# Optimization experiments

Measured on AMD Instinct MI355X. Metric: run time of the kernel, lower is better.

The kernel has to match this reference:

```python
import jax, jax.numpy as jnp
import numpy as np


def setup_inputs() -> dict:
    key = jax.random.key(0)
    ks = jax.random.split(key, 6)
    B, S, D, F, E = 4, 2048, 512, 2048, 8
    scale = 0.02
    return {
        "x": jax.random.normal(ks[0], (B, S, D), dtype=jnp.float32),
        "gate_w": jax.random.normal(ks[1], (D, E), dtype=jnp.float32) * scale,
        "w1": jax.random.normal(ks[2], (E, D, F), dtype=jnp.float32) * scale,
        "b1": jax.random.normal(ks[3], (E, F), dtype=jnp.float32) * scale,
        "w2": jax.random.normal(ks[4], (E, F, D), dtype=jnp.float32) * scale,
        "b2": jax.random.normal(ks[5], (E, D), dtype=jnp.float32) * scale,
    }


TOP_K = 2


def reference(x, gate_w, w1, b1, w2, b2):
    E = w1.shape[0]
    orig_shape = x.shape
    xr = x.reshape(-1, x.shape[-1])              # [T, D]

    # Router
    logits = xr @ gate_w                          # [T, E]
    probs = jax.nn.softmax(logits, axis=-1)
    mean_probs = probs.mean(axis=0)               # [E]
    load_balance_loss = E * jnp.sum(mean_probs * mean_probs)

    topw, topi = jax.lax.top_k(probs, TOP_K)      # [T, K]
    topw = topw / jnp.sum(topw, axis=-1, keepdims=True)

    # Per-token combine weight per expert: sum over top-k slots of weight * one-hot
    combine = jnp.sum(jax.nn.one_hot(topi, E, dtype=xr.dtype) * topw[..., None], axis=1)  # [T, E]

    # Dense per-expert FFN (equivalent math to the permute/slice dispatch:
    # each selected token gets expert_e(x) scaled by its normalized router weight).
    hidden = jax.nn.gelu(jnp.einsum("td,edf->etf", xr, w1) + b1[:, None, :], approximate=False)  # [E, T, F]
    outs = jnp.einsum("etf,efd->etd", hidden, w2) + b2[:, None, :]                               # [E, T, D]

    y = jnp.einsum("etd,te->td", outs, combine)   # [T, D]
    return y.reshape(orig_shape), load_balance_loss
```

## Files before the change

### kernel.cpp

```cpp
#include <hip/hip_runtime.h>
#include <stdint.h>

#define T_TOKENS 8192
#define D_DIM 512
#define F_DIM 2048
#define E_NUM 8

typedef short short8 __attribute__((ext_vector_type(8)));
typedef float f32x4 __attribute__((ext_vector_type(4)));

__device__ __forceinline__ unsigned short f2bf(float f) {
    union { float f; unsigned int u; } c; c.f = f;
    unsigned int u = c.u;
    unsigned int r = (u + 0x7fffu + ((u >> 16) & 1u)) >> 16;
    return (unsigned short)r;
}
__device__ __forceinline__ unsigned int pack2(float a, float b) {
    return (unsigned int)f2bf(a) | ((unsigned int)f2bf(b) << 16);
}
__device__ __forceinline__ float gelu_fast(float h) {
    float a = h * fmaf(h * h, -0.0713548162f, -1.5957691216f);
    return h / (1.f + __expf(a));
}

#define SLOT_CAP 17408
#define WS_COUNT 0
#define WS_PROBS 512
#define WS_TOK   16384
#define WS_WGT   (WS_TOK + E_NUM * T_TOKENS * 4)
#define WS_W1B   (1ull << 20)
#define WS_W2B   (WS_W1B + 16777216ull)
#define WS_XG    (WS_W2B + 16777216ull)
#define WS_HG    (WS_XG + (unsigned long long)SLOT_CAP * D_DIM * 2)

__device__ __forceinline__ void expert_off(const int* __restrict__ count, int e,
                                           int& off_e, int& cnt_e) {
    int off = 0, ce = 0;
#pragma unroll
    for (int i = 0; i < E_NUM; ++i) {
        int c = count[i];
        if (i == e) ce = c;
        if (i < e) off += (c + 127) & ~127;
    }
    off_e = off; cnt_e = ce;
}

__global__ __launch_bounds__(256) void moe_pre(
    const float* __restrict__ w1, const float* __restrict__ w2,
    const float* __restrict__ x,  const float* __restrict__ gw,
    unsigned short* __restrict__ w1b, unsigned short* __restrict__ w2b,
    int* __restrict__ count, float* __restrict__ probs_g,
    int* __restrict__ tok_list, float* __restrict__ wgt_list,
    float* __restrict__ y)
{
    int tid = threadIdx.x;

    if (blockIdx.x < 8192) {
        __shared__ float ts[32][65];
        {
            size_t gid = (size_t)blockIdx.x * 256 + tid;
            ((float2*)y)[gid] = make_float2(0.f, 0.f);
        }
        if (blockIdx.x == 0 && tid < E_NUM) { count[tid] = 0; probs_g[tid] = 0.f; }

        int b = blockIdx.x;
        bool is2 = b >= 4096;
        int o = is2 ? b - 4096 : b;
        int e = o >> 9, r = o & 511;
        int N  = is2 ? 512 : 2048;
        int Ks = is2 ? 64 : 16;
        int ng, ks;
        if (!is2) { ng = r & 31; ks = r >> 5; }
        else      { ng = r & 7;  ks = r >> 3; }

        const float* src = (is2 ? w2 : w1) + ((size_t)e << 20) + (size_t)(ks * 32) * N + ng * 64;
        int row = tid >> 3, c4 = (tid & 7) * 4;
        f32x4 v0 = *(const f32x4*)(src + (size_t)row * N + c4);
        f32x4 v1 = *(const f32x4*)(src + (size_t)row * N + c4 + 32);
        *(f32x4*)&ts[row][c4] = v0;
        *(f32x4*)&ts[row][c4 + 32] = v1;
        __syncthreads();

        int f = tid >> 6, L = tid & 63, q = L >> 4, n = L & 15;
        float v[8];
#pragma unroll
        for (int j = 0; j < 8; ++j) v[j] = ts[q * 8 + j][f * 16 + n];
        uint4 pk;
        pk.x = pack2(v[0], v[1]); pk.y = pack2(v[2], v[3]);
        pk.z = pack2(v[4], v[5]); pk.w = pack2(v[6], v[7]);
        size_t fraglane = ((size_t)((e * (N / 16) + ng * 4 + f) * Ks + ks)) * 64 + L;
        unsigned short* dst = (is2 ? w2b : w1b) + fraglane * 8;
        *(uint4*)dst = pk;
        return;
    }

    int rbx = blockIdx.x - 8192;
    __shared__ float pprob[E_NUM];
    __shared__ int   lcnt[E_NUM];
    __shared__ int   gbase[E_NUM];
    __shared__ int   ltok[E_NUM][64];
    __shared__ float lwgt[E_NUM][64];

    if (tid < E_NUM) { pprob[tid] = 0.f; lcnt[tid] = 0; }
    __syncthreads();

    int wv = tid >> 6, lane = tid & 63;

    float gr[64];
    {
        const f32x4* gp = (const f32x4*)(gw + lane * 64);
#pragma unroll
        for (int i = 0; i < 16; ++i) *(f32x4*)&gr[i * 4] = gp[i];
    }

    float wps[E_NUM];
#pragma unroll
    for (int e = 0; e < E_NUM; ++e) wps[e] = 0.f;

#pragma unroll 1
    for (int i = 0; i < 8; ++i) {
        int t = rbx * 32 + wv * 8 + i;
        const float* xp = x + (size_t)t * D_DIM + lane * 8;
        f32x4 x0 = *(const f32x4*)xp;
        f32x4 x1 = *(const f32x4*)(xp + 4);
        float xv[8] = { x0.x, x0.y, x0.z, x0.w, x1.x, x1.y, x1.z, x1.w };
        float acc[E_NUM];
#pragma unroll
        for (int e = 0; e < E_NUM; ++e) acc[e] = 0.f;
#pragma unroll
        for (int j = 0; j < 8; ++j)
#pragma unroll
            for (int e = 0; e < E_NUM; ++e) acc[e] += xv[j] * gr[j * 8 + e];
#pragma unroll
        for (int off = 1; off < 64; off <<= 1)
#pragma unroll
            for (int e = 0; e < E_NUM; ++e) acc[e] += __shfl_xor(acc[e], off);

        float m = acc[0];
#pragma unroll
        for (int e = 1; e < E_NUM; ++e) m = fmaxf(m, acc[e]);
        float p[E_NUM], s = 0.f;
#pragma unroll
        for (int e = 0; e < E_NUM; ++e) { p[e] = __expf(acc[e] - m); s += p[e]; }
        float inv = 1.f / s;
#pragma unroll
        for (int e = 0; e < E_NUM; ++e) { p[e] *= inv; wps[e] += p[e]; }

        int e1 = 0;
#pragma unroll
        for (int e = 1; e < E_NUM; ++e) if (p[e] > p[e1]) e1 = e;
        int e2 = (e1 == 0) ? 1 : 0;
#pragma unroll
        for (int e = 0; e < E_NUM; ++e) if (e != e1 && p[e] > p[e2]) e2 = e;

        if (lane == 0) {
            float invw = 1.f / (p[e1] + p[e2]);
            int s1 = atomicAdd(&lcnt[e1], 1); ltok[e1][s1] = t; lwgt[e1][s1] = p[e1] * invw;
            int s2 = atomicAdd(&lcnt[e2], 1); ltok[e2][s2] = t; lwgt[e2][s2] = p[e2] * invw;
        }
    }
    if (lane == 0) {
#pragma unroll
        for (int e = 0; e < E_NUM; ++e) atomicAdd(&pprob[e], wps[e]);
    }
    __syncthreads();
    if (tid < E_NUM) {
        gbase[tid] = atomicAdd(&count[tid], lcnt[tid]);
        atomicAdd(&probs_g[tid], pprob[tid]);
    }
    __syncthreads();
    int ee = tid >> 5;
    for (int ss = tid & 31; ss < lcnt[ee]; ss += 32) {
        int dst = ee * T_TOKENS + gbase[ee] + ss;
        tok_list[dst] = ltok[ee][ss];
        wgt_list[dst] = lwgt[ee][ss];
    }
}

__global__ __launch_bounds__(256) void moe_gather(
    const float* __restrict__ x, const int* __restrict__ count,
    const int* __restrict__ tok_list, unsigned short* __restrict__ Xg,
    const float* __restrict__ probs_g, float* __restrict__ y)
{
    if (blockIdx.x == 0 && threadIdx.x == 0) {
        float s = 0.f;
#pragma unroll
        for (int i = 0; i < E_NUM; ++i) {
            float m = probs_g[i] / (float)T_TOKENS;
            s += m * m;
        }
        y[(size_t)T_TOKENS * D_DIM] = (float)E_NUM * s;
    }

    int e = blockIdx.x & 7, tile = blockIdx.x >> 3;
    int off_e, cnt;
    expert_off(count, e, off_e, cnt);
    int padcnt = (cnt + 127) & ~127;
    if (tile * 64 >= padcnt) return;

    int tid = threadIdx.x;
    int tl = tid >> 2;
    int kq = tid & 3;
    int slot = tile * 64 + tl;
    bool valid = slot < cnt;
    int tok = valid ? tok_list[e * T_TOKENS + slot] : 0;
    const float* xr = x + (size_t)tok * D_DIM + kq * 128;
    int base16 = ((off_e + tile * 64) >> 4) + (tl >> 4);
    int mlane = tl & 15;

#pragma unroll 4
    for (int g = 0; g < 16; ++g) {
        uint4 pk;
        if (valid) {
            f32x4 v0 = *(const f32x4*)(xr + g * 8);
            f32x4 v1 = *(const f32x4*)(xr + g * 8 + 4);
            pk.x = pack2(v0.x, v0.y); pk.y = pack2(v0.z, v0.w);
            pk.z = pack2(v1.x, v1.y); pk.w = pack2(v1.z, v1.w);
        } else {
            pk.x = 0; pk.y = 0; pk.z = 0; pk.w = 0;
        }
        int kb = kq * 4 + (g >> 2);
        int lane = mlane + 16 * (g & 3);
        *(uint4*)(Xg + ((size_t)(base16 * 16 + kb) * 64 + lane) * 8) = pk;
    }
}

__global__ __launch_bounds__(256) void moe_gemm1(
    const unsigned short* __restrict__ Xg, const unsigned short* __restrict__ w1b,
    const float* __restrict__ b1, const int* __restrict__ count,
    unsigned short* __restrict__ Hg)
{
    int e = blockIdx.x & 7;
    int r = blockIdx.x >> 3;
    int mt = r >> 4, nt = r & 15;
    int off_e, cnt;
    expert_off(count, e, off_e, cnt);
    if (mt * 128 >= cnt) return;

    __shared__ unsigned short us[4][64][72];

    int tid = threadIdx.x;
    int wv = tid >> 6, lane = tid & 63;
    int wh = wv >> 1, nh = wv & 1;
    int q = lane >> 4, n = lane & 15;

    int slot16b = (off_e >> 4) + mt * 8 + wh * 4;
    const short8* Ap = (const short8*)Xg + (size_t)slot16b * 1024 + lane;
    const short8* Bp = (const short8*)w1b + (size_t)(e * 128 + nt * 8 + nh * 4) * 1024 + lane;

    f32x4 acc[4][4];
#pragma unroll
    for (int j = 0; j < 4; ++j)
#pragma unroll
        for (int i = 0; i < 4; ++i) acc[j][i] = (f32x4){0.f, 0.f, 0.f, 0.f};

#pragma unroll 1
    for (int ks = 0; ks < 16; ks += 4) {
        short8 A[4][4], B[4][4];
#pragma unroll
        for (int u = 0; u < 4; ++u) {
#pragma unroll
            for (int i = 0; i < 4; ++i) A[u][i] = Ap[(size_t)i * 1024 + (ks + u) * 64];
#pragma unroll
            for (int j = 0; j < 4; ++j) B[u][j] = Bp[(size_t)j * 1024 + (ks + u) * 64];
        }
#pragma unroll
        for (int u = 0; u < 4; ++u)
#pragma unroll
            for (int j = 0; j < 4; ++j)
#pragma unroll
                for (int i = 0; i < 4; ++i)
                    acc[j][i] = __builtin_amdgcn_mfma_f32_16x16x32_bf16(A[u][i], B[u][j], acc[j][i], 0, 0, 0);
    }

#pragma unroll
    for (int j = 0; j < 4; ++j) {
        float bb = b1[e * F_DIM + (nt * 8 + nh * 4 + j) * 16 + n];
#pragma unroll
        for (int i = 0; i < 4; ++i)
#pragma unroll
            for (int rr = 0; rr < 4; ++rr)
                us[wv][i * 16 + q * 4 + rr][j * 16 + n] = f2bf(gelu_fast(acc[j][i][rr] + bb));
    }
    __syncthreads();

#pragma unroll
    for (int i = 0; i < 4; ++i)
#pragma unroll
        for (int kb = 0; kb < 2; ++kb) {
            short8 v = *(const short8*)&us[wv][i * 16 + n][kb * 32 + q * 8];
            size_t idx = ((size_t)(slot16b + i) * 64 + (nt * 4 + nh * 2 + kb)) * 64 + lane;
            *(short8*)((unsigned short*)Hg + idx * 8) = v;
        }
}

__global__ __launch_bounds__(256) void moe_gemm2(
    const unsigned short* __restrict__ Hg, const unsigned short* __restrict__ w2b,
    const float* __restrict__ b2, const int* __restrict__ count,
    const int* __restrict__ tok_list, const float* __restrict__ wgt_list,
    float* __restrict__ y)
{
    int e = blockIdx.x & 7;
    int r = blockIdx.x >> 3;
    int mt = r >> 2, nt = r & 3;
    int off_e, cnt;
    expert_off(count, e, off_e, cnt);
    if (mt * 128 >= cnt) return;

    __shared__ int   stok[128];
    __shared__ float swgt[128];

    int tid = threadIdx.x;
    if (tid < 128) {
        int s = mt * 128 + tid;
        if (s < cnt) { stok[tid] = tok_list[e * T_TOKENS + s]; swgt[tid] = wgt_list[e * T_TOKENS + s]; }
        else         { stok[tid] = 0; swgt[tid] = 0.f; }
    }
    __syncthreads();

    int wv = tid >> 6, lane = tid & 63;
    int wh = wv >> 1, nh = wv & 1;
    int q = lane >> 4, n = lane & 15;

    int slot16b = (off_e >> 4) + mt * 8 + wh * 4;
    const short8* Ap = (const short8*)Hg + (size_t)slot16b * 4096 + lane;
    const short8* Bp = (const short8*)w2b + (size_t)(e * 32 + nt * 8 + nh * 4) * 4096 + lane;

    f32x4 acc[4][4];
#pragma unroll
    for (int j = 0; j < 4; ++j)
#pragma unroll
        for (int i = 0; i < 4; ++i) acc[j][i] = (f32x4){0.f, 0.f, 0.f, 0.f};

#pragma unroll 1
    for (int kb = 0; kb < 64; kb += 4) {
        short8 A[4][4], B[4][4];
#pragma unroll
        for (int u = 0; u < 4; ++u) {
#pragma unroll
            for (int i = 0; i < 4; ++i) A[u][i] = Ap[(size_t)i * 4096 + (kb + u) * 64];
#pragma unroll
            for (int j = 0; j < 4; ++j) B[u][j] = Bp[(size_t)j * 4096 + (kb + u) * 64];
        }
#pragma unroll
        for (int u = 0; u < 4; ++u)
#pragma unroll
            for (int j = 0; j < 4; ++j)
#pragma unroll
                for (int i = 0; i < 4; ++i)
                    acc[j][i] = __builtin_amdgcn_mfma_f32_16x16x32_bf16(A[u][i], B[u][j], acc[j][i], 0, 0, 0);
    }

#pragma unroll
    for (int j = 0; j < 4; ++j) {
        int d = (nt * 8 + nh * 4 + j) * 16 + n;
        float bb = b2[e * D_DIM + d];
#pragma unroll
        for (int i = 0; i < 4; ++i)
#pragma unroll
            for (int rr = 0; rr < 4; ++rr) {
                int m = wh * 64 + i * 16 + q * 4 + rr;
                float wg = swgt[m];
                if (wg != 0.f)
                    atomicAdd(y + (size_t)stok[m] * D_DIM + d, wg * (acc[j][i][rr] + bb));
            }
    }
}

extern "C" void kernel_launch(void* const* d_in, const int* in_sizes, int n_in,
                              void* d_out, int out_size, void* d_ws, size_t ws_size,
                              hipStream_t stream) {
    const float* x  = (const float*)d_in[0];
    const float* gw = (const float*)d_in[1];
    const float* w1 = (const float*)d_in[2];
    const float* b1 = (const float*)d_in[3];
    const float* w2 = (const float*)d_in[4];
    const float* b2 = (const float*)d_in[5];
    float* out = (float*)d_out;

    char* ws = (char*)d_ws;
    int*   count     = (int*)(ws + WS_COUNT);
    float* probs_g   = (float*)(ws + WS_PROBS);
    int*   tok_list  = (int*)(ws + WS_TOK);
    float* wgt_list  = (float*)(ws + WS_WGT);
    unsigned short* w1b = (unsigned short*)(ws + WS_W1B);
    unsigned short* w2b = (unsigned short*)(ws + WS_W2B);
    unsigned short* Xg  = (unsigned short*)(ws + WS_XG);
    unsigned short* Hg  = (unsigned short*)(ws + WS_HG);

    moe_pre<<<8192 + T_TOKENS / 32, 256, 0, stream>>>(
        w1, w2, x, gw, w1b, w2b, count, probs_g, tok_list, wgt_list, out);
    moe_gather<<<8 * 128, 256, 0, stream>>>(x, count, tok_list, Xg, probs_g, out);
    moe_gemm1<<<8 * 64 * 16, 256, 0, stream>>>(Xg, w1b, b1, count, Hg);
    moe_gemm2<<<8 * 64 * 4, 256, 0, stream>>>(Hg, w2b, b2, count, tok_list, wgt_list, out);
}
```

Measured before the change: 328.9 us.

## Stage GEMM2 operand tiles in LDS via direct global-to-LDS loads

The second expert GEMM no longer has every wave load its A and B fragments straight from global memory into registers. Each k-step, two waves copy the 128-row Hg tile and the other two copy the 128-column w2 tile into shared memory with global_load_lds. All four waves then read their fragments from LDS. This halves redundant global traffic, since fragments are shared across wave pairs, but it adds two block barriers per step with no double buffering, so load latency is no longer overlapped with MFMA.

New measurement: 326.9 us. About the same (-0.6%).

```diff
diff --git a/kernel.cpp b/kernel.cpp
--- a/kernel.cpp
+++ b/kernel.cpp
@@ -21,6 +21,11 @@
 __device__ __forceinline__ float gelu_fast(float h) {
     float a = h * fmaf(h * h, -0.0713548162f, -1.5957691216f);
     return h / (1.f + __expf(a));
+}
+__device__ __forceinline__ void gload_lds16(const unsigned short* g, unsigned short* l) {
+    __builtin_amdgcn_global_load_lds(
+        (const __attribute__((address_space(1))) void*)g,
+        (__attribute__((address_space(3))) void*)l, 16, 0, 0);
 }
 
 #define SLOT_CAP 17408
@@ -307,6 +312,8 @@
     expert_off(count, e, off_e, cnt);
     if (mt * 128 >= cnt) return;
 
+    __shared__ __align__(16) unsigned short As[2][8][512];
+    __shared__ __align__(16) unsigned short Bs[2][8][512];
     __shared__ int   stok[128];
     __shared__ float swgt[128];
 
@@ -316,15 +323,14 @@
         if (s < cnt) { stok[tid] = tok_list[e * T_TOKENS + s]; swgt[tid] = wgt_list[e * T_TOKENS + s]; }
         else         { stok[tid] = 0; swgt[tid] = 0.f; }
     }
-    __syncthreads();
 
     int wv = tid >> 6, lane = tid & 63;
     int wh = wv >> 1, nh = wv & 1;
     int q = lane >> 4, n = lane & 15;
 
-    int slot16b = (off_e >> 4) + mt * 8 + wh * 4;
-    const short8* Ap = (const short8*)Hg + (size_t)slot16b * 4096 + lane;
-    const short8* Bp = (const short8*)w2b + (size_t)(e * 32 + nt * 8 + nh * 4) * 4096 + lane;
+    int slot16b = (off_e >> 4) + mt * 8;
+    const short8* HgS = (const short8*)Hg;
+    const short8* W2S = (const short8*)w2b;
 
     f32x4 acc[4][4];
 #pragma unroll
@@ -333,22 +339,40 @@
         for (int i = 0; i < 4; ++i) acc[j][i] = (f32x4){0.f, 0.f, 0.f, 0.f};
 
 #pragma unroll 1
-    for (int kb = 0; kb < 64; kb += 4) {
-        short8 A[4][4], B[4][4];
-#pragma unroll
-        for (int u = 0; u < 4; ++u) {
-#pragma unroll
-            for (int i = 0; i < 4; ++i) A[u][i] = Ap[(size_t)i * 4096 + (kb + u) * 64];
-#pragma unroll
-            for (int j = 0; j < 4; ++j) B[u][j] = Bp[(size_t)j * 4096 + (kb + u) * 64];
-        }
-#pragma unroll
-        for (int u = 0; u < 4; ++u)
+    for (int s = 0; s < 32; ++s) {
+        int k0 = s * 2;
+        if (wv < 2) {
+            int u = wv;
+#pragma unroll
+            for (int i = 0; i < 8; ++i) {
+                const unsigned short* g = (const unsigned short*)
+                    (HgS + ((size_t)(slot16b + i) * 64 + (k0 + u)) * 64 + lane);
+                gload_lds16(g, &As[u][i][0]);
+            }
+        } else {
+            int u = wv - 2;
+#pragma unroll
+            for (int i = 0; i < 8; ++i) {
+                const unsigned short* g = (const unsigned short*)
+                    (W2S + ((size_t)((e * 32 + nt * 8 + i) * 64) + (k0 + u)) * 64 + lane);
+                gload_lds16(g, &Bs[u][i][0]);
+            }
+        }
+        __syncthreads();
+#pragma unroll
+        for (int u = 0; u < 2; ++u) {
+            short8 A[4], B[4];
+#pragma unroll
+            for (int i = 0; i < 4; ++i) A[i] = *(const short8*)&As[u][wh * 4 + i][lane * 8];
+#pragma unroll
+            for (int j = 0; j < 4; ++j) B[j] = *(const short8*)&Bs[u][nh * 4 + j][lane * 8];
 #pragma unroll
             for (int j = 0; j < 4; ++j)
 #pragma unroll
                 for (int i = 0; i < 4; ++i)
-                    acc[j][i] = __builtin_amdgcn_mfma_f32_16x16x32_bf16(A[u][i], B[u][j], acc[j][i], 0, 0, 0);
+                    acc[j][i] = __builtin_amdgcn_mfma_f32_16x16x32_bf16(A[i], B[j], acc[j][i], 0, 0, 0);
+        }
+        __syncthreads();
     }
 
 #pragma unroll
```
